# Performance work log

Hardware: AMD Instinct MI355X
Metric: run time of the kernel (lower is better)

The kernel has to match this reference:

```python
import jax, jax.numpy as jnp
import numpy as np

B, S, H = 4, 2048, 1024
NH, HD = 16, 64  # num heads, head dim
NUM_TASKS = 8


def setup_inputs() -> dict:
    key = jax.random.key(0)
    ks = jax.random.split(key, 12)
    sc = 1.0 / np.sqrt(H)
    return {
        "hidden_states": jax.random.normal(ks[0], (B, S, H), dtype=jnp.float32),
        "attention_mask": jnp.zeros((B, 1, 1, S), dtype=jnp.float32),
        "Wq": jax.random.normal(ks[1], (H, H), dtype=jnp.float32) * sc,
        "bq": jnp.zeros((H,), dtype=jnp.float32),
        "Wk": jax.random.normal(ks[2], (H, H), dtype=jnp.float32) * sc,
        "bk": jnp.zeros((H,), dtype=jnp.float32),
        "Wv": jax.random.normal(ks[3], (H, H), dtype=jnp.float32) * sc,
        "bv": jnp.zeros((H,), dtype=jnp.float32),
        "q_emb": jax.random.normal(ks[4], (NUM_TASKS, H), dtype=jnp.float32) * 0.02,
        "k_emb": jax.random.normal(ks[5], (NUM_TASKS, H), dtype=jnp.float32) * 0.02,
        "v_emb": jax.random.normal(ks[6], (NUM_TASKS, H), dtype=jnp.float32) * 0.02,
        "index": 3,
    }


def _split_heads(x):
    # [B,S,H] -> [B,NH,S,HD]
    b, s, _ = x.shape
    return x.reshape(b, s, NH, HD).transpose(0, 2, 1, 3)


def reference(hidden_states, attention_mask, Wq, bq, Wk, bk, Wv, bv,
              q_emb, k_emb, v_emb, index):
    # projections + per-task additive bias (broadcast over batch and seq)
    q = hidden_states @ Wq + bq + q_emb[index][None, None, :]
    k = hidden_states @ Wk + bk + k_emb[index][None, None, :]
    v = hidden_states @ Wv + bv + v_emb[index][None, None, :]

    q = _split_heads(q)  # [B,NH,S,HD]
    k = _split_heads(k)
    v = _split_heads(v)

    scores = jnp.einsum("bhqd,bhkd->bhqk", q, k) / np.sqrt(HD)
    scores = scores + attention_mask  # additive mask broadcasts [B,1,1,S]
    probs = jax.nn.softmax(scores, axis=-1)  # dropout prob 0 -> identity

    ctx = jnp.einsum("bhqk,bhkd->bhqd", probs, v)
    ctx = ctx.transpose(0, 2, 1, 3).reshape(hidden_states.shape[0], -1, H)
    return ctx
```

## Files before the change

kernel.cpp:

```cpp
#include <hip/hip_runtime.h>
#include <hip/hip_bf16.h>
#include <stdint.h>

#define BB 4
#define SS 2048
#define HH 1024
#define NHH 16
#define HDD 64
#define M_TOT (BB*SS)

#define XB_OFF 0
#define WT_OFF (M_TOT*HH)
#define Q_OFF  (WT_OFF + 3*HH*HH)
#define K_OFF  (Q_OFF + BB*NHH*SS*HDD)
#define VT_OFF (K_OFF + BB*NHH*SS*HDD)

typedef short bf16x8 __attribute__((ext_vector_type(8)));
typedef float f32x4  __attribute__((ext_vector_type(4)));

__device__ inline unsigned short f2bf(float f){
  unsigned u = __float_as_uint(f);
  u += 0x7fffu + ((u >> 16) & 1u);
  return (unsigned short)(u >> 16);
}
__device__ inline unsigned pk2bf(float lo, float hi){
  float2 t; t.x = lo; t.y = hi;
  __hip_bfloat162 h = __float22bfloat162_rn(t);
  return *(unsigned*)&h;
}

__device__ __forceinline__ void ld_g2l_16(const unsigned short* g, unsigned short* l){
  __builtin_amdgcn_global_load_lds(
      (const __attribute__((address_space(1))) void*)g,
      (__attribute__((address_space(3))) void*)l, 16, 0, 0);
}

__global__ void convert_x(const float* __restrict__ hs, unsigned short* __restrict__ xb){
  const int i = blockIdx.x*blockDim.x + threadIdx.x;
  float4 v = ((const float4*)hs)[i];
  ushort4 o;
  o.x = f2bf(v.x); o.y = f2bf(v.y); o.z = f2bf(v.z); o.w = f2bf(v.w);
  ((ushort4*)xb)[i] = o;
}

__global__ void convert_wt(const float* __restrict__ wq, const float* __restrict__ wk,
                           const float* __restrict__ wv, unsigned short* __restrict__ wt){
  __shared__ unsigned short t[64][65];
  const int z = blockIdx.z;
  const float* W = (z==0) ? wq : ((z==1) ? wk : wv);
  unsigned short* WT = wt + z*HH*HH;
  const int kb = blockIdx.x*64, nb = blockIdx.y*64;
  const int tid = threadIdx.x;
  #pragma unroll
  for (int i = 0; i < 16; i++){
    const int idx = i*256 + tid;
    const int r = idx >> 6, c = idx & 63;
    t[r][c] = f2bf(W[(kb + r)*HH + nb + c]);
  }
  __syncthreads();
  #pragma unroll
  for (int i = 0; i < 16; i++){
    const int idx = i*256 + tid;
    const int n = idx >> 6, k = idx & 63;
    WT[(nb + n)*HH + kb + k] = t[k][n];
  }
}

__global__ __launch_bounds__(256) void qkv_gemm(
    const unsigned short* __restrict__ ws16, unsigned short* __restrict__ wsq,
    const float* __restrict__ bq, const float* __restrict__ bk, const float* __restrict__ bv,
    const float* __restrict__ qe, const float* __restrict__ ke, const float* __restrict__ ve,
    const int* __restrict__ idxp){
  __shared__ unsigned short al[128*32];
  __shared__ unsigned short bl[128*32];

  const unsigned short* Xb = ws16 + XB_OFF;
  const int z = blockIdx.z;
  const unsigned short* Wt = ws16 + WT_OFF + z*HH*HH;
  const float* bias = (z==0) ? bq : ((z==1) ? bk : bv);
  const float* emb  = (z==0) ? qe : ((z==1) ? ke : ve);

  const int tid  = threadIdx.x;
  const int wv   = tid >> 6;
  const int ln   = tid & 63;
  const int quad = ln >> 4;
  const int l15  = ln & 15;
  const int m0 = blockIdx.x * 128;
  const int n0 = blockIdx.y * 128;
  const int wm = wv & 1, wn = wv >> 1;

  const int sr0 = wv*32 + (ln >> 2);
  const int sr1 = sr0 + 16;
  const int sk  = (ln & 3)*8;
  const unsigned short* ga0 = &Xb[(size_t)(m0 + sr0)*HH + sk];
  const unsigned short* ga1 = &Xb[(size_t)(m0 + sr1)*HH + sk];
  const unsigned short* gb0 = &Wt[(size_t)(n0 + sr0)*HH + sk];
  const unsigned short* gb1 = &Wt[(size_t)(n0 + sr1)*HH + sk];
  unsigned short* alb0 = &al[wv*1024];
  unsigned short* alb1 = &al[wv*1024 + 512];
  unsigned short* blb0 = &bl[wv*1024];
  unsigned short* blb1 = &bl[wv*1024 + 512];

  f32x4 acc[4][4] = {};

  for (int k0 = 0; k0 < HH; k0 += 32){
    __syncthreads();
    ld_g2l_16(ga0 + k0, alb0);
    ld_g2l_16(ga1 + k0, alb1);
    ld_g2l_16(gb0 + k0, blb0);
    ld_g2l_16(gb1 + k0, blb1);
    __syncthreads();

    bf16x8 af[4], bf[4];
    #pragma unroll
    for (int i = 0; i < 4; i++){
      af[i] = *(const bf16x8*)&al[(wm*64 + i*16 + l15)*32 + quad*8];
      bf[i] = *(const bf16x8*)&bl[(wn*64 + i*16 + l15)*32 + quad*8];
    }
    #pragma unroll
    for (int mi = 0; mi < 4; mi++)
      #pragma unroll
      for (int ni = 0; ni < 4; ni++)
        acc[mi][ni] = __builtin_amdgcn_mfma_f32_16x16x32_bf16(af[mi], bf[ni], acc[mi][ni], 0, 0, 0);
  }

  const int index = idxp[0];
  const float oscale = (z==0) ? 0.18033688011112042f : 1.0f;
  #pragma unroll
  for (int ni = 0; ni < 4; ni++){
    const int n = n0 + wn*64 + ni*16 + l15;
    const float biasv = bias[n] + emb[index*HH + n];
    const int h = n >> 6, d = n & 63;
    #pragma unroll
    for (int mi = 0; mi < 4; mi++){
      #pragma unroll
      for (int r = 0; r < 4; r++){
        const int g  = m0 + wm*64 + mi*16 + quad*4 + r;
        const int b_ = g >> 11;
        const int s_ = g & (SS - 1);
        const int bh = b_*NHH + h;
        const unsigned short val = f2bf((acc[mi][ni][r] + biasv) * oscale);
        if (z == 2)      wsq[VT_OFF + (size_t)(bh*HDD + d)*SS + s_] = val;
        else if (z == 0) wsq[Q_OFF  + (size_t)(bh*SS + s_)*HDD + d] = val;
        else             wsq[K_OFF  + (size_t)(bh*SS + s_)*HDD + d] = val;
      }
    }
  }
}

#define ST_P 40
__global__ __launch_bounds__(512, 6) void attn_mfma(
    const unsigned short* __restrict__ ws16,
    const float* __restrict__ mask, float* __restrict__ out){
  __shared__ __align__(16) unsigned short kb[2][32*64];
  __shared__ __align__(16) unsigned short vb[2][64*32];
  __shared__ __align__(16) unsigned short pb[8][16*ST_P];
  __shared__ __align__(16) float mlds[SS];

  const int tid  = threadIdx.x;
  const int wave = tid >> 6;
  const int lane = tid & 63;
  const int quad = lane >> 4;
  const int l15  = lane & 15;

  const int bid  = (blockIdx.x & 7)*128 + (blockIdx.x >> 3);
  const int qb   = bid & 15;
  const int bh   = bid >> 4;
  const int b    = bh >> 4, h = bh & 15;
  const int q0   = qb*128 + wave*16;
  const float LOG2E = 1.4426950408889634f;

  const unsigned short* Qg = ws16 + Q_OFF  + (size_t)bh*SS*HDD;
  const unsigned short* Kg = ws16 + K_OFF  + (size_t)bh*SS*HDD;
  const unsigned short* Vg = ws16 + VT_OFF + (size_t)bh*HDD*SS;
  const float* maskB = mask + b*SS;

  {
    float4 m4 = ((const float4*)maskB)[tid];
    m4.x*=LOG2E; m4.y*=LOG2E; m4.z*=LOG2E; m4.w*=LOG2E;
    *(float4*)&mlds[tid*4] = m4;
  }

  bf16x8 aq[2];
  #pragma unroll
  for (int h2 = 0; h2 < 2; h2++)
    aq[h2] = *(const bf16x8*)(Qg + (size_t)(q0 + l15)*HDD + h2*32 + quad*8);

  const unsigned short* sSrc;
  unsigned short* sDst;
  int sAdv;
  if (tid < 256){
    const int kr = tid >> 3, kp = tid & 7;
    sSrc = Kg + (size_t)kr*HDD + ((((kp*16) ^ ((kr&7)<<4)))>>1);
    sDst = &kb[0][0] + tid*8;
    sAdv = 32*HDD;
  } else {
    const int t = tid - 256;
    const int vr = t >> 2, vp = t & 3;
    sSrc = Vg + (size_t)vr*SS + vp*8;
    sDst = &vb[0][0] + t*8;
    sAdv = 32;
  }
  unsigned short* pw = &pb[wave][0];

  f32x4 O[4] = {};
  float lacc = 0.f;

  ld_g2l_16(sSrc, sDst);
  const unsigned short* sp = sSrc + sAdv;
  __syncthreads();

  #pragma unroll 2
  for (int ch = 0; ch < 64; ++ch){
    const int cur = ch & 1;
    const int ktb = ch*32;
    if (ch < 63){
      ld_g2l_16(sp, sDst + (cur^1)*2048);
      sp += sAdv;
    }
    const unsigned short* kcur = &kb[cur][0];
    const unsigned short* vcur = &vb[cur][0];

    bf16x8 ka[2][2];
    #pragma unroll
    for (int fi = 0; fi < 2; fi++)
      #pragma unroll
      for (int h2 = 0; h2 < 2; h2++){
        const int colb = (h2*64 + quad*16) ^ ((l15 & 7) << 4);
        ka[fi][h2] = *(const bf16x8*)&kcur[(fi*16 + l15)*64 + (colb>>1)];
      }

    #pragma unroll
    for (int fi = 0; fi < 2; fi++){
      f32x4 st = *(const f32x4*)&mlds[ktb + fi*16 + quad*4];
      st = __builtin_amdgcn_mfma_f32_16x16x32_bf16(ka[fi][0], aq[0], st, 0,0,0);
      st = __builtin_amdgcn_mfma_f32_16x16x32_bf16(ka[fi][1], aq[1], st, 0,0,0);
      f32x4 p;
      #pragma unroll
      for (int r = 0; r < 4; r++) p[r] = __builtin_amdgcn_exp2f(st[r]);
      lacc += (p[0] + p[1]) + (p[2] + p[3]);
      uint2 w; w.x = pk2bf(p[0], p[1]); w.y = pk2bf(p[2], p[3]);
      *(uint2*)&pw[l15*ST_P + fi*16 + quad*4] = w;
    }

    bf16x8 va[4];
    #pragma unroll
    for (int dg = 0; dg < 4; dg++)
      va[dg] = *(const bf16x8*)&vcur[(dg*16 + l15)*32 + quad*8];

    {
      bf16x8 bp = *(const bf16x8*)&pw[l15*ST_P + quad*8];
      #pragma unroll
      for (int dg = 0; dg < 4; dg++)
        O[dg] = __builtin_amdgcn_mfma_f32_16x16x32_bf16(va[dg], bp, O[dg], 0,0,0);
    }

    __syncthreads();
  }

  float lq = lacc;
  lq += __shfl_xor(lq, 16);
  lq += __shfl_xor(lq, 32);
  const float inv = 1.0f / lq;

  float* op = out + ((size_t)b*SS + q0 + l15)*HH + h*HDD + quad*4;
  #pragma unroll
  for (int dg = 0; dg < 4; dg++){
    f32x4 v = O[dg];
    float4 o; o.x = v[0]*inv; o.y = v[1]*inv; o.z = v[2]*inv; o.w = v[3]*inv;
    *(float4*)(op + dg*16) = o;
  }
}

extern "C" void kernel_launch(void* const* d_in, const int* in_sizes, int n_in,
                              void* d_out, int out_size, void* d_ws, size_t ws_size,
                              hipStream_t stream){
  const float* hs   = (const float*)d_in[0];
  const float* mask = (const float*)d_in[1];
  const float* Wq   = (const float*)d_in[2];
  const float* bq   = (const float*)d_in[3];
  const float* Wk   = (const float*)d_in[4];
  const float* bk   = (const float*)d_in[5];
  const float* Wv   = (const float*)d_in[6];
  const float* bv   = (const float*)d_in[7];
  const float* qe   = (const float*)d_in[8];
  const float* ke   = (const float*)d_in[9];
  const float* ve   = (const float*)d_in[10];
  const int*   idx  = (const int*)d_in[11];
  unsigned short* ws16 = (unsigned short*)d_ws;
  float* out = (float*)d_out;

  convert_x<<<M_TOT*HH/4/256, 256, 0, stream>>>(hs, ws16 + XB_OFF);
  dim3 gt(HH/64, HH/64, 3);
  convert_wt<<<gt, 256, 0, stream>>>(Wq, Wk, Wv, ws16 + WT_OFF);

  dim3 g2(M_TOT/128, HH/128, 3);
  qkv_gemm<<<g2, 256, 0, stream>>>(ws16, ws16, bq, bk, bv, qe, ke, ve, idx);

  attn_mfma<<<BB*NHH*SS/128, 512, 0, stream>>>(ws16, mask, out);
}
```

Measured before the change: 292.6 us.

## Vectorize projection epilogue stores via operand swap; add MFMA priority hints in attention

For the Q and K projections, the MFMA operands are swapped so each lane holds four consecutive head-dim values. The epilogue can then write ushort4 vectors with float4 bias loads instead of scattered scalar 2-byte stores. The V-transpose path also packs four consecutive sequence positions into one ushort4 store. In the attention kernel, V fragment loads are hoisted ahead of the score MFMAs, s_setprio brackets the MFMA groups, and the occupancy hint in launch_bounds is dropped, which may change register allocation and occupancy.

```diff
diff --git a/kernel.cpp b/kernel.cpp
--- a/kernel.cpp
+++ b/kernel.cpp
@@ -117,39 +117,70 @@
       af[i] = *(const bf16x8*)&al[(wm*64 + i*16 + l15)*32 + quad*8];
       bf[i] = *(const bf16x8*)&bl[(wn*64 + i*16 + l15)*32 + quad*8];
     }
-    #pragma unroll
-    for (int mi = 0; mi < 4; mi++)
-      #pragma unroll
-      for (int ni = 0; ni < 4; ni++)
-        acc[mi][ni] = __builtin_amdgcn_mfma_f32_16x16x32_bf16(af[mi], bf[ni], acc[mi][ni], 0, 0, 0);
+    if (z == 2){
+      #pragma unroll
+      for (int mi = 0; mi < 4; mi++)
+        #pragma unroll
+        for (int ni = 0; ni < 4; ni++)
+          acc[mi][ni] = __builtin_amdgcn_mfma_f32_16x16x32_bf16(af[mi], bf[ni], acc[mi][ni], 0, 0, 0);
+    } else {
+      #pragma unroll
+      for (int mi = 0; mi < 4; mi++)
+        #pragma unroll
+        for (int ni = 0; ni < 4; ni++)
+          acc[mi][ni] = __builtin_amdgcn_mfma_f32_16x16x32_bf16(bf[ni], af[mi], acc[mi][ni], 0, 0, 0);
+    }
   }
 
   const int index = idxp[0];
-  const float oscale = (z==0) ? 0.18033688011112042f : 1.0f;
-  #pragma unroll
-  for (int ni = 0; ni < 4; ni++){
-    const int n = n0 + wn*64 + ni*16 + l15;
-    const float biasv = bias[n] + emb[index*HH + n];
-    const int h = n >> 6, d = n & 63;
-    #pragma unroll
-    for (int mi = 0; mi < 4; mi++){
-      #pragma unroll
-      for (int r = 0; r < 4; r++){
-        const int g  = m0 + wm*64 + mi*16 + quad*4 + r;
+  if (z == 2){
+    #pragma unroll
+    for (int ni = 0; ni < 4; ni++){
+      const int n = n0 + wn*64 + ni*16 + l15;
+      const float biasv = bias[n] + emb[index*HH + n];
+      const int h = n >> 6, d = n & 63;
+      #pragma unroll
+      for (int mi = 0; mi < 4; mi++){
+        const int g  = m0 + wm*64 + mi*16 + quad*4;
         const int b_ = g >> 11;
         const int s_ = g & (SS - 1);
         const int bh = b_*NHH + h;
-        const unsigned short val = f2bf((acc[mi][ni][r] + biasv) * oscale);
-        if (z == 2)      wsq[VT_OFF + (size_t)(bh*HDD + d)*SS + s_] = val;
-        else if (z == 0) wsq[Q_OFF  + (size_t)(bh*SS + s_)*HDD + d] = val;
-        else             wsq[K_OFF  + (size_t)(bh*SS + s_)*HDD + d] = val;
+        const f32x4 a = acc[mi][ni];
+        ushort4 o;
+        o.x = f2bf(a[0] + biasv); o.y = f2bf(a[1] + biasv);
+        o.z = f2bf(a[2] + biasv); o.w = f2bf(a[3] + biasv);
+        *(ushort4*)&wsq[VT_OFF + (size_t)(bh*HDD + d)*SS + s_] = o;
       }
     }
+  } else {
+    const float oscale = (z==0) ? 0.18033688011112042f : 1.0f;
+    const size_t obase = (z==0) ? (size_t)Q_OFF : (size_t)K_OFF;
+    #pragma unroll
+    for (int mi = 0; mi < 4; mi++){
+      const int sg = m0 + wm*64 + mi*16 + l15;
+      const int b_ = sg >> 11;
+      const int s_ = sg & (SS - 1);
+      #pragma unroll
+      for (int ni = 0; ni < 4; ni++){
+        const int nb = n0 + wn*64 + ni*16 + quad*4;
+        const int h  = nb >> 6, d0 = nb & 63;
+        const int bh = b_*NHH + h;
+        const float4 b4 = *(const float4*)&bias[nb];
+        const float4 e4 = *(const float4*)&emb[index*HH + nb];
+        const f32x4 a = acc[mi][ni];
+        ushort4 o;
+        o.x = f2bf((a[0] + b4.x + e4.x) * oscale);
+        o.y = f2bf((a[1] + b4.y + e4.y) * oscale);
+        o.z = f2bf((a[2] + b4.z + e4.z) * oscale);
+        o.w = f2bf((a[3] + b4.w + e4.w) * oscale);
+        *(ushort4*)&wsq[obase + (size_t)(bh*SS + s_)*HDD + d0] = o;
+      }
+    }
   }
 }
 
 #define ST_P 40
-__global__ __launch_bounds__(512, 6) void attn_mfma(
+__global__ __launch_bounds__(512) void attn_mfma(
     const unsigned short* __restrict__ ws16,
     const float* __restrict__ mask, float* __restrict__ out){
   __shared__ __align__(16) unsigned short kb[2][32*64];
@@ -221,6 +252,11 @@
     const unsigned short* kcur = &kb[cur][0];
     const unsigned short* vcur = &vb[cur][0];
 
+    bf16x8 va[4];
+    #pragma unroll
+    for (int dg = 0; dg < 4; dg++)
+      va[dg] = *(const bf16x8*)&vcur[(dg*16 + l15)*32 + quad*8];
+
     bf16x8 ka[2][2];
     #pragma unroll
     for (int fi = 0; fi < 2; fi++)
@@ -233,8 +269,10 @@
     #pragma unroll
     for (int fi = 0; fi < 2; fi++){
       f32x4 st = *(const f32x4*)&mlds[ktb + fi*16 + quad*4];
+      __builtin_amdgcn_s_setprio(1);
       st = __builtin_amdgcn_mfma_f32_16x16x32_bf16(ka[fi][0], aq[0], st, 0,0,0);
       st = __builtin_amdgcn_mfma_f32_16x16x32_bf16(ka[fi][1], aq[1], st, 0,0,0);
+      __builtin_amdgcn_s_setprio(0);
       f32x4 p;
       #pragma unroll
       for (int r = 0; r < 4; r++) p[r] = __builtin_amdgcn_exp2f(st[r]);
@@ -243,16 +281,13 @@
       *(uint2*)&pw[l15*ST_P + fi*16 + quad*4] = w;
     }
 
-    bf16x8 va[4];
-    #pragma unroll
-    for (int dg = 0; dg < 4; dg++)
-      va[dg] = *(const bf16x8*)&vcur[(dg*16 + l15)*32 + quad*8];
-
     {
       bf16x8 bp = *(const bf16x8*)&pw[l15*ST_P + quad*8];
+      __builtin_amdgcn_s_setprio(1);
       #pragma unroll
       for (int dg = 0; dg < 4; dg++)
         O[dg] = __builtin_amdgcn_mfma_f32_16x16x32_bf16(va[dg], bp, O[dg], 0,0,0);
+      __builtin_amdgcn_s_setprio(0);
     }
 
     __syncthreads();
```

New measurement: 340.2 us. 1.16x slower.
